# Optimization experiments

Hardware: AMD Instinct MI355X
Metric: run time of the kernel (lower is better)

The kernel has to match this reference:

```python
import jax, jax.numpy as jnp
import numpy as np

U = I = 100000  # user/item vocab (set equal; __init__ swaps them anyway)
P = 50          # position_len
D = 64          # hidden_units_u == hidden_units_i
B = 8192        # batch
H = 50          # history length


def _attn(data, key, W, b):
    # data: [B,D], key: [B,H,D]; Linear(2D,1) -> Tanh -> Softmax over H
    attn_in = jnp.concatenate([jnp.broadcast_to(data[:, None, :], key.shape), key], axis=-1)  # [B,H,2D]
    w = jax.nn.softmax(jnp.tanh(attn_in @ W + b), axis=1)  # [B,H,1]
    return jnp.sum(w * key, axis=1)  # [B,D]


def setup_inputs() -> dict:
    key = jax.random.key(0)
    ks = jax.random.split(key, 24)
    emb = lambda i, shape: jax.random.normal(ks[i], shape, jnp.float32) * 0.05
    uni = lambda i, shape: jax.random.uniform(ks[i], shape, jnp.float32, -1.0, 1.0)
    ri = lambda i, shape, hi: jax.random.randint(ks[i], shape, 0, hi, jnp.int32)
    return {
        "user1": ri(0, (B,), U), "item1": ri(1, (B,), I),
        "user2": ri(2, (B,), U), "item2": ri(3, (B,), I),
        "u_his": ri(4, (B, H), I), "u_pos": ri(5, (B, H), P), "u_his_mask": ri(6, (B, H), 2),
        "i_his": ri(7, (B, H), U), "i_pos": ri(8, (B, H), P), "i_his_mask": ri(9, (B, H), 2),
        "user1_emb": emb(10, (U, D)), "item1_emb": emb(11, (I, D)),
        "user1_bias": uni(12, (U,)), "item1_bias": uni(13, (I,)),
        "u_pos_emb": emb(14, (P, D)),
        "user2_emb": emb(15, (U, D)), "item2_emb": emb(16, (I, D)),
        "user2_bias": uni(17, (U,)), "item2_bias": uni(18, (I,)),
        "i_pos_emb": emb(19, (P, D)),
        "attn_u_W": emb(20, (2 * D, 1)), "attn_u_b": emb(21, (1,)),
        "attn_i_W": emb(22, (2 * D, 1)), "attn_i_b": emb(23, (1,)),
    }


def _forward(user1_emb, item1_emb, user1_bias, item1_bias, u_pos_emb,
             user2_emb, item2_emb, user2_bias, item2_bias, i_pos_emb,
             attn_u_W, attn_u_b, attn_i_W, attn_i_b,
             user1, item1, user2, item2,
             u_his, u_pos, u_his_mask, i_his, i_pos, i_his_mask):
    sg = jax.lax.stop_gradient
    mu = (u_his_mask != 0).astype(jnp.float32)[..., None]  # [B,H,1]
    mi = (i_his_mask != 0).astype(jnp.float32)[..., None]

    # branch 1 (shared-sign s, detached r)
    u1s = user1_emb[user1]; i1s = item1_emb[item1]
    u1s_b = user1_bias[user1]; i1s_b = item1_bias[item1]
    u1r = sg(user2_emb[user1]); i1r = sg(item2_emb[item1])
    u1r_b = sg(user2_bias[user1]); i1r_b = sg(item2_bias[item1])
    u_hiss = item1_emb[u_his] * mu            # [B,H,D], masked-zero
    i_hisr = sg(user2_emb[i_his]) * mi
    u_poss = u_pos_emb[u_pos] * mu
    i_posr = sg(i_pos_emb[i_pos]) * mi
    u_ds = _attn(i1s, u_hiss + u_poss, attn_u_W, attn_u_b)
    i_dr = _attn(u1r, i_hisr + i_posr, attn_i_W, attn_i_b)
    logits_us = u1s_b + i1s_b + jnp.sum((u_ds + i1s) * u1s, axis=1)
    logits_ir = u1r_b + i1r_b + jnp.sum((i_dr + i1r) * u1r, axis=1)

    # branch 2 (roles swapped)
    u2s = user2_emb[user2]; i2s = item2_emb[item2]
    u2s_b = user2_bias[user2]; i2s_b = item2_bias[item2]
    u2r = sg(user1_emb[user2]); i2r = sg(item1_emb[item2])
    u2r_b = sg(user1_bias[user2]); i2r_b = sg(item1_bias[item2])
    u_hisr = sg(item1_emb[u_his]) * mu
    i_hiss = user2_emb[i_his] * mi
    u_posr = sg(u_pos_emb[u_pos]) * mu
    i_poss = i_pos_emb[i_pos] * mi
    u_dr = _attn(i1r, u_hisr + u_posr, attn_u_W, attn_u_b)
    i_ds = _attn(u1s, i_hiss + i_poss, attn_i_W, attn_i_b)
    logits_ur = u2r_b + i2r_b + jnp.sum((u_dr + i2r) * u2r, axis=1)
    logits_is = u2s_b + i2s_b + jnp.sum((i_ds + i2s) * u2s, axis=1)

    loss_reg1 = jnp.sum(u1s ** 2) + jnp.sum(i1s ** 2) + jnp.sum(u_hiss ** 2)
    loss_reg2 = jnp.sum(u2s ** 2) + jnp.sum(i2s ** 2) + jnp.sum(i_hiss ** 2)
    return (logits_us, logits_ir, logits_ur, logits_is, loss_reg1, loss_reg2)


def reference(user1, item1, user2, item2, u_his, u_pos, u_his_mask, i_his, i_pos, i_his_mask,
              user1_emb, item1_emb, user1_bias, item1_bias, u_pos_emb,
              user2_emb, item2_emb, user2_bias, item2_bias, i_pos_emb,
              attn_u_W, attn_u_b, attn_i_W, attn_i_b):
    return _forward(user1_emb, item1_emb, user1_bias, item1_bias, u_pos_emb,
                    user2_emb, item2_emb, user2_bias, item2_bias, i_pos_emb,
                    attn_u_W, attn_u_b, attn_i_W, attn_i_b,
                    user1, item1, user2, item2,
                    u_his, u_pos, u_his_mask, i_his, i_pos, i_his_mask)
```

## Files before the change

### kernel.cpp

```cpp
#include <hip/hip_runtime.h>

#define NB 8192
#define NH 50
#define ND 64

__device__ __forceinline__ float wsum(float v) {
#pragma unroll
    for (int o = 32; o > 0; o >>= 1) v += __shfl_xor(v, o, 64);
    return v;
}

__device__ __forceinline__ float tanh_fast(float x) {
    const float e = __expf(2.0f * x);
    return (e - 1.0f) * __builtin_amdgcn_rcpf(e + 1.0f);
}

__global__ __launch_bounds__(256, 8) void kw_kernel(
    const float* __restrict__ t0, const float* __restrict__ t1,
    const float* __restrict__ t2, const float* __restrict__ t3,
    const float* __restrict__ w0, const float* __restrict__ w1,
    const float* __restrict__ w2, const float* __restrict__ w3,
    float* __restrict__ o0, float* __restrict__ o1,
    float* __restrict__ o2, float* __restrict__ o3,
    int r0, int r1, int r2, int r3,
    int b1, int b2, int b3)
{
    const int blk = blockIdx.x;
    const float* tab; const float* W; float* o; int rows, base;
    if (blk < b1)      { tab = t0; W = w0; o = o0; rows = r0; base = blk; }
    else if (blk < b2) { tab = t1; W = w1; o = o1; rows = r1; base = blk - b1; }
    else if (blk < b3) { tab = t2; W = w2; o = o2; rows = r2; base = blk - b2; }
    else               { tab = t3; W = w3; o = o3; rows = r3; base = blk - b3; }
    const int lane = threadIdx.x & 63;
    const int wv = threadIdx.x >> 6;
    const int sub = lane >> 4, j = lane & 15;
    const int row = base * 16 + wv * 4 + sub;
    const int rowc = min(row, rows - 1);
    const float4 v = *(const float4*)(tab + (size_t)rowc * ND + j * 4);
    const float4 w = *(const float4*)(W + j * 4);
    float p = v.x * w.x + v.y * w.y + v.z * w.z + v.w * w.w;
    p += __shfl_xor(p, 1, 64);
    p += __shfl_xor(p, 2, 64);
    p += __shfl_xor(p, 4, 64);
    p += __shfl_xor(p, 8, 64);
    if (j == 0 && row < rows) o[row] = p;
}

__global__ __launch_bounds__(256, 8) void fwd_kernel(
    const int* __restrict__ user1, const int* __restrict__ item1,
    const int* __restrict__ user2, const int* __restrict__ item2,
    const int* __restrict__ u_his, const int* __restrict__ u_pos, const int* __restrict__ u_mask,
    const int* __restrict__ i_his, const int* __restrict__ i_pos, const int* __restrict__ i_mask,
    const float* __restrict__ user1_emb, const float* __restrict__ item1_emb,
    const float* __restrict__ user1_bias, const float* __restrict__ item1_bias,
    const float* __restrict__ u_pos_emb,
    const float* __restrict__ user2_emb, const float* __restrict__ item2_emb,
    const float* __restrict__ user2_bias, const float* __restrict__ item2_bias,
    const float* __restrict__ i_pos_emb,
    const float* __restrict__ attn_u_W, const float* __restrict__ attn_u_b,
    const float* __restrict__ attn_i_W, const float* __restrict__ attn_i_b,
    const float* __restrict__ KWu, const float* __restrict__ KWi,
    const float* __restrict__ PWu, const float* __restrict__ PWi,
    float* __restrict__ out, float* __restrict__ ws)
{
    const int wave = threadIdx.x >> 6;
    const int d = threadIdx.x & 63;
    const int b = __builtin_amdgcn_readfirstlane(blockIdx.x * 2 + (wave >> 1));
    const bool iw = (wave & 1);

    const int iu1 = user1[b], ii1 = item1[b], iu2 = user2[b], ii2 = item2[b];

    const int*   his  = iw ? i_his  : u_his;
    const int*   posa = iw ? i_pos  : u_pos;
    const int*   msk  = iw ? i_mask : u_mask;
    const float* ktab = iw ? user2_emb : item1_emb;
    const float* ptab = iw ? i_pos_emb : u_pos_emb;
    const float* W    = iw ? attn_i_W  : attn_u_W;
    const float  bb   = iw ? attn_i_b[0] : attn_u_b[0];
    const float* KW   = iw ? KWi : KWu;
    const float* PW   = iw ? PWi : PWu;

    int hidx = 0, hpos = 0;
    bool act = false;
    if (d < NH) {
        hidx = his[b * NH + d];
        hpos = posa[b * NH + d];
        act  = (msk[b * NH + d] != 0);
    }
    const float s = KW[hidx] + PW[hpos];

    const float* qa_tab = iw ? user2_emb : item1_emb;
    const float* qb_tab = iw ? user1_emb : item2_emb;
    const int    qidx   = iw ? iu1 : ii1;
    const float qa = qa_tab[(size_t)qidx * ND + d];
    const float qb = qb_tab[(size_t)qidx * ND + d];
    const float pa    = iw ? item2_emb[(size_t)ii1 * ND + d] : user1_emb[(size_t)iu1 * ND + d];
    const float add_b = (iw ? item2_emb : item1_emb)[(size_t)ii2 * ND + d];
    const float mul_b = (iw ? user2_emb : user1_emb)[(size_t)iu2 * ND + d];

    const float Wq = W[d];
    const float cq_a = wsum(qa * Wq) + bb;
    const float cq_b = wsum(qb * Wq) + bb;
    const float e0_a = __expf(tanh_fast(cq_a));
    const float e0_b = __expf(tanh_fast(cq_b));

    float e_a = 0.0f, e_b = 0.0f;
    if (d < NH) {
        e_a = act ? __expf(tanh_fast(cq_a + s)) : e0_a;
        e_b = act ? __expf(tanh_fast(cq_b + s)) : e0_b;
    }
    const float den_a = wsum(e_a);
    const float den_b = wsum(e_b);

    const unsigned long long bal = __ballot(act);
    const int nact = __builtin_amdgcn_readfirstlane(__popcll(bal));
    const int below = __builtin_amdgcn_mbcnt_hi(
        (unsigned)(bal >> 32), __builtin_amdgcn_mbcnt_lo((unsigned)bal, 0));
    const int tgt = (act ? below : 63) << 2;
    const int idx_c = __builtin_amdgcn_ds_permute(tgt, hidx);
    const int pos_c = __builtin_amdgcn_ds_permute(tgt, hpos);
    const int ea_c  = __builtin_amdgcn_ds_permute(tgt, __float_as_int(e_a));
    const int eb_c  = __builtin_amdgcn_ds_permute(tgt, __float_as_int(e_b));

    float o_a = 0.0f, o_b = 0.0f, reg = 0.0f;
#pragma unroll 8
    for (int h = 0; h < nact; ++h) {
        const int ih = __builtin_amdgcn_readlane(idx_c, h);
        const int ip = __builtin_amdgcn_readlane(pos_c, h);
        const float ea = __int_as_float(__builtin_amdgcn_readlane(ea_c, h));
        const float eb = __int_as_float(__builtin_amdgcn_readlane(eb_c, h));
        const float kv = ktab[(size_t)ih * ND + d];
        const float pv = ptab[ip * ND + d];
        const float k = kv + pv;
        o_a += ea * k;
        o_b += eb * k;
        reg += kv * kv;
    }
    o_a *= __builtin_amdgcn_rcpf(den_a);
    o_b *= __builtin_amdgcn_rcpf(den_b);

    const float add_a = iw ? pa : qa;
    const float mul_a = iw ? qa : pa;
    const float l_a = wsum((o_a + add_a) * mul_a);
    const float l_b = wsum((o_b + add_b) * mul_b);
    const float rv = iw ? (mul_b * mul_b + add_b * add_b) : (mul_a * mul_a + qa * qa);
    const float r = wsum(rv + reg);

    const float* ub = iw ? user2_bias : user1_bias;
    const float* ib = iw ? item2_bias : item1_bias;
    if (d == 0) {
        out[(iw ? NB : 0) + b]          = ub[iu1] + ib[ii1] + l_a;
        out[(iw ? 3 * NB : 2 * NB) + b] = ub[iu2] + ib[ii2] + l_b;
        ws[(iw ? NB : 0) + b] = r;
    }
}

__global__ __launch_bounds__(256, 8) void fwd_fallback(
    const int* __restrict__ user1, const int* __restrict__ item1,
    const int* __restrict__ user2, const int* __restrict__ item2,
    const int* __restrict__ u_his, const int* __restrict__ u_pos, const int* __restrict__ u_mask,
    const int* __restrict__ i_his, const int* __restrict__ i_pos, const int* __restrict__ i_mask,
    const float* __restrict__ user1_emb, const float* __restrict__ item1_emb,
    const float* __restrict__ user1_bias, const float* __restrict__ item1_bias,
    const float* __restrict__ u_pos_emb,
    const float* __restrict__ user2_emb, const float* __restrict__ item2_emb,
    const float* __restrict__ user2_bias, const float* __restrict__ item2_bias,
    const float* __restrict__ i_pos_emb,
    const float* __restrict__ attn_u_W, const float* __restrict__ attn_u_b,
    const float* __restrict__ attn_i_W, const float* __restrict__ attn_i_b,
    float* __restrict__ out, float* __restrict__ ws)
{
    const int wave = threadIdx.x >> 6;
    const int d = threadIdx.x & 63;
    const int b = __builtin_amdgcn_readfirstlane(blockIdx.x * 2 + (wave >> 1));
    const bool iw = (wave & 1);

    const int iu1 = user1[b], ii1 = item1[b], iu2 = user2[b], ii2 = item2[b];
    const int*   his  = iw ? i_his  : u_his;
    const int*   posa = iw ? i_pos  : u_pos;
    const int*   msk  = iw ? i_mask : u_mask;
    const float* ktab = iw ? user2_emb : item1_emb;
    const float* ptab = iw ? i_pos_emb : u_pos_emb;
    const float* W    = iw ? attn_i_W  : attn_u_W;
    const float  bb   = iw ? attn_i_b[0] : attn_u_b[0];
    const float* qa_tab = iw ? user2_emb : item1_emb;
    const float* qb_tab = iw ? user1_emb : item2_emb;
    const int    qidx   = iw ? iu1 : ii1;
    const float qa = qa_tab[(size_t)qidx * ND + d];
    const float qb = qb_tab[(size_t)qidx * ND + d];
    const float Wq = W[d], Wk = W[ND + d];
    const float cq_a = wsum(qa * Wq) + bb;
    const float cq_b = wsum(qb * Wq) + bb;

    int hidx = 0, hpos = 0;
    bool act = false;
    if (d < NH) {
        hidx = his[b * NH + d];
        hpos = posa[b * NH + d];
        act  = (msk[b * NH + d] != 0);
    }
    const unsigned long long bal = __ballot(act);
    const int nact = __builtin_amdgcn_readfirstlane(__popcll(bal));
    const int below = __builtin_amdgcn_mbcnt_hi(
        (unsigned)(bal >> 32), __builtin_amdgcn_mbcnt_lo((unsigned)bal, 0));
    const int tgt = (act ? below : 63) << 2;
    const int idx_c = __builtin_amdgcn_ds_permute(tgt, hidx);
    const int pos_c = __builtin_amdgcn_ds_permute(tgt, hpos);

    float o_a = 0.0f, o_b = 0.0f, den_a = 0.0f, den_b = 0.0f, reg = 0.0f;
#pragma unroll 4
    for (int h = 0; h < nact; ++h) {
        const int ih = __builtin_amdgcn_readlane(idx_c, h);
        const int ip = __builtin_amdgcn_readlane(pos_c, h);
        const float kv = ktab[(size_t)ih * ND + d];
        const float pv = ptab[(size_t)ip * ND + d];
        const float k = kv + pv;
        reg += kv * kv;
        const float s = wsum(k * Wk);
        const float ea = __expf(tanh_fast(cq_a + s));
        const float eb = __expf(tanh_fast(cq_b + s));
        o_a += ea * k;  den_a += ea;
        o_b += eb * k;  den_b += eb;
    }
    den_a += (float)(NH - nact) * __expf(tanh_fast(cq_a));
    den_b += (float)(NH - nact) * __expf(tanh_fast(cq_b));
    o_a *= __builtin_amdgcn_rcpf(den_a);
    o_b *= __builtin_amdgcn_rcpf(den_b);

    const float pa = iw ? item2_emb[(size_t)ii1 * ND + d] : user1_emb[(size_t)iu1 * ND + d];
    const float add_a = iw ? pa : qa;
    const float mul_a = iw ? qa : pa;
    const float add_b = (iw ? item2_emb : item1_emb)[(size_t)ii2 * ND + d];
    const float mul_b = (iw ? user2_emb : user1_emb)[(size_t)iu2 * ND + d];
    const float l_a = wsum((o_a + add_a) * mul_a);
    const float l_b = wsum((o_b + add_b) * mul_b);
    const float rv = iw ? (mul_b * mul_b + add_b * add_b) : (mul_a * mul_a + qa * qa);
    const float r = wsum(rv + reg);
    const float* ub = iw ? user2_bias : user1_bias;
    const float* ib = iw ? item2_bias : item1_bias;
    if (d == 0) {
        out[(iw ? NB : 0) + b]          = ub[iu1] + ib[ii1] + l_a;
        out[(iw ? 3 * NB : 2 * NB) + b] = ub[iu2] + ib[ii2] + l_b;
        ws[(iw ? NB : 0) + b] = r;
    }
}

__global__ void reduce_kernel(const float* __restrict__ ws, float* __restrict__ out) {
    float a = 0.0f, c = 0.0f;
    for (int i = threadIdx.x; i < NB; i += 256) {
        a += ws[i];
        c += ws[NB + i];
    }
    a = wsum(a);
    c = wsum(c);
    __shared__ float sa[4], sc[4];
    const int w = threadIdx.x >> 6, d = threadIdx.x & 63;
    if (d == 0) { sa[w] = a; sc[w] = c; }
    __syncthreads();
    if (threadIdx.x == 0) {
        out[4 * NB]     = sa[0] + sa[1] + sa[2] + sa[3];
        out[4 * NB + 1] = sc[0] + sc[1] + sc[2] + sc[3];
    }
}

extern "C" void kernel_launch(void* const* d_in, const int* in_sizes, int n_in,
                              void* d_out, int out_size, void* d_ws, size_t ws_size,
                              hipStream_t stream) {
    const int* user1 = (const int*)d_in[0];
    const int* item1 = (const int*)d_in[1];
    const int* user2 = (const int*)d_in[2];
    const int* item2 = (const int*)d_in[3];
    const int* u_his = (const int*)d_in[4];
    const int* u_pos = (const int*)d_in[5];
    const int* u_msk = (const int*)d_in[6];
    const int* i_his = (const int*)d_in[7];
    const int* i_pos = (const int*)d_in[8];
    const int* i_msk = (const int*)d_in[9];
    const float* user1_emb  = (const float*)d_in[10];
    const float* item1_emb  = (const float*)d_in[11];
    const float* user1_bias = (const float*)d_in[12];
    const float* item1_bias = (const float*)d_in[13];
    const float* u_pos_emb  = (const float*)d_in[14];
    const float* user2_emb  = (const float*)d_in[15];
    const float* item2_emb  = (const float*)d_in[16];
    const float* user2_bias = (const float*)d_in[17];
    const float* item2_bias = (const float*)d_in[18];
    const float* i_pos_emb  = (const float*)d_in[19];
    const float* attn_u_W = (const float*)d_in[20];
    const float* attn_u_b = (const float*)d_in[21];
    const float* attn_i_W = (const float*)d_in[22];
    const float* attn_i_b = (const float*)d_in[23];
    float* out = (float*)d_out;
    float* ws  = (float*)d_ws;

    const int I_rows = in_sizes[11] / ND;
    const int U_rows = in_sizes[15] / ND;
    const int P_rows = in_sizes[14] / ND;

    float* KWu = ws + 2 * NB;
    float* KWi = KWu + I_rows;
    float* PWu = KWi + U_rows;
    float* PWi = PWu + 64;
    const size_t need = (size_t)(2 * NB + I_rows + U_rows + 128) * sizeof(float);

    if (ws_size >= need) {
        const int nb0 = (I_rows + 15) / 16;
        const int nb1 = (U_rows + 15) / 16;
        const int nb2 = (P_rows + 15) / 16;
        const int b1 = nb0, b2 = nb0 + nb1, b3 = nb0 + nb1 + nb2;
        const int total = b3 + nb2;
        kw_kernel<<<total, 256, 0, stream>>>(
            item1_emb, user2_emb, u_pos_emb, i_pos_emb,
            attn_u_W + ND, attn_i_W + ND, attn_u_W + ND, attn_i_W + ND,
            KWu, KWi, PWu, PWi,
            I_rows, U_rows, P_rows, P_rows,
            b1, b2, b3);
        fwd_kernel<<<NB / 2, 256, 0, stream>>>(
            user1, item1, user2, item2,
            u_his, u_pos, u_msk, i_his, i_pos, i_msk,
            user1_emb, item1_emb, user1_bias, item1_bias, u_pos_emb,
            user2_emb, item2_emb, user2_bias, item2_bias, i_pos_emb,
            attn_u_W, attn_u_b, attn_i_W, attn_i_b,
            KWu, KWi, PWu, PWi,
            out, ws);
    } else {
        fwd_fallback<<<NB / 2, 256, 0, stream>>>(
            user1, item1, user2, item2,
            u_his, u_pos, u_msk, i_his, i_pos, i_msk,
            user1_emb, item1_emb, user1_bias, item1_bias, u_pos_emb,
            user2_emb, item2_emb, user2_bias, item2_bias, i_pos_emb,
            attn_u_W, attn_u_b, attn_i_W, attn_i_b,
            out, ws);
    }
    reduce_kernel<<<1, 256, 0, stream>>>(ws, out);
}
```

Before: 210.0 us.

## Split history gather across two waves per attention branch with LDS reduction

Each block now handles one batch row instead of two. Two waves share each attention branch, and each wave gathers half of the active history entries. Partial weighted sums and regularization terms are combined through shared memory after a block barrier, and the first wave finishes the logits. This shortens each wave's serial gather chain to raise memory-level parallelism, at the cost of twice as many blocks, redundant per-wave setup work (index loads, softmax denominators) and a __syncthreads.

```diff
diff --git a/kernel.cpp b/kernel.cpp
--- a/kernel.cpp
+++ b/kernel.cpp
@@ -65,8 +65,10 @@
 {
     const int wave = threadIdx.x >> 6;
     const int d = threadIdx.x & 63;
-    const int b = __builtin_amdgcn_readfirstlane(blockIdx.x * 2 + (wave >> 1));
-    const bool iw = (wave & 1);
+    const int b = __builtin_amdgcn_readfirstlane(blockIdx.x);
+    const bool iw = (wave >> 1);
+    const int half = wave & 1;
+    const int pair = wave >> 1;
 
     const int iu1 = user1[b], ii1 = item1[b], iu2 = user2[b], ii2 = item2[b];
 
@@ -94,9 +96,13 @@
     const int    qidx   = iw ? iu1 : ii1;
     const float qa = qa_tab[(size_t)qidx * ND + d];
     const float qb = qb_tab[(size_t)qidx * ND + d];
-    const float pa    = iw ? item2_emb[(size_t)ii1 * ND + d] : user1_emb[(size_t)iu1 * ND + d];
-    const float add_b = (iw ? item2_emb : item1_emb)[(size_t)ii2 * ND + d];
-    const float mul_b = (iw ? user2_emb : user1_emb)[(size_t)iu2 * ND + d];
+
+    float pa = 0.0f, add_b = 0.0f, mul_b = 0.0f;
+    if (half == 0) {
+        pa    = iw ? item2_emb[(size_t)ii1 * ND + d] : user1_emb[(size_t)iu1 * ND + d];
+        add_b = (iw ? item2_emb : item1_emb)[(size_t)ii2 * ND + d];
+        mul_b = (iw ? user2_emb : user1_emb)[(size_t)iu2 * ND + d];
+    }
 
     const float Wq = W[d];
     const float cq_a = wsum(qa * Wq) + bb;
@@ -122,9 +128,12 @@
     const int ea_c  = __builtin_amdgcn_ds_permute(tgt, __float_as_int(e_a));
     const int eb_c  = __builtin_amdgcn_ds_permute(tgt, __float_as_int(e_b));
 
+    const int h_lo = half ? (nact >> 1) : 0;
+    const int h_hi = half ? nact : (nact >> 1);
+
     float o_a = 0.0f, o_b = 0.0f, reg = 0.0f;
 #pragma unroll 8
-    for (int h = 0; h < nact; ++h) {
+    for (int h = h_lo; h < h_hi; ++h) {
         const int ih = __builtin_amdgcn_readlane(idx_c, h);
         const int ip = __builtin_amdgcn_readlane(pos_c, h);
         const float ea = __int_as_float(__builtin_amdgcn_readlane(ea_c, h));
@@ -136,22 +145,36 @@
         o_b += eb * k;
         reg += kv * kv;
     }
-    o_a *= __builtin_amdgcn_rcpf(den_a);
-    o_b *= __builtin_amdgcn_rcpf(den_b);
-
-    const float add_a = iw ? pa : qa;
-    const float mul_a = iw ? qa : pa;
-    const float l_a = wsum((o_a + add_a) * mul_a);
-    const float l_b = wsum((o_b + add_b) * mul_b);
-    const float rv = iw ? (mul_b * mul_b + add_b * add_b) : (mul_a * mul_a + qa * qa);
-    const float r = wsum(rv + reg);
-
-    const float* ub = iw ? user2_bias : user1_bias;
-    const float* ib = iw ? item2_bias : item1_bias;
-    if (d == 0) {
-        out[(iw ? NB : 0) + b]          = ub[iu1] + ib[ii1] + l_a;
-        out[(iw ? 3 * NB : 2 * NB) + b] = ub[iu2] + ib[ii2] + l_b;
-        ws[(iw ? NB : 0) + b] = r;
+
+    __shared__ float s_oa[2][ND], s_ob[2][ND], s_reg[2];
+    if (half == 1) {
+        s_oa[pair][d] = o_a;
+        s_ob[pair][d] = o_b;
+        if (d == 0) s_reg[pair] = 0.0f;
+    }
+    const float reg_half = wsum(reg);
+    if (half == 1 && d == 0) s_reg[pair] = reg_half;
+    __syncthreads();
+    if (half == 0) {
+        o_a += s_oa[pair][d];
+        o_b += s_ob[pair][d];
+        o_a *= __builtin_amdgcn_rcpf(den_a);
+        o_b *= __builtin_amdgcn_rcpf(den_b);
+
+        const float add_a = iw ? pa : qa;
+        const float mul_a = iw ? qa : pa;
+        const float l_a = wsum((o_a + add_a) * mul_a);
+        const float l_b = wsum((o_b + add_b) * mul_b);
+        const float rv = iw ? (mul_b * mul_b + add_b * add_b) : (mul_a * mul_a + qa * qa);
+        const float r = wsum(rv) + reg_half + s_reg[pair];
+
+        const float* ub = iw ? user2_bias : user1_bias;
+        const float* ib = iw ? item2_bias : item1_bias;
+        if (d == 0) {
+            out[(iw ? NB : 0) + b]          = ub[iu1] + ib[ii1] + l_a;
+            out[(iw ? 3 * NB : 2 * NB) + b] = ub[iu2] + ib[ii2] + l_b;
+            ws[(iw ? NB : 0) + b] = r;
+        }
     }
 }
 
@@ -315,7 +338,7 @@
             KWu, KWi, PWu, PWi,
             I_rows, U_rows, P_rows, P_rows,
             b1, b2, b3);
-        fwd_kernel<<<NB / 2, 256, 0, stream>>>(
+        fwd_kernel<<<NB, 256, 0, stream>>>(
             user1, item1, user2, item2,
             u_his, u_pos, u_msk, i_his, i_pos, i_msk,
             user1_emb, item1_emb, user1_bias, item1_bias, u_pos_emb,
```

Measured after the change: 218.8 us. 1.04x slower.
